# Optimization experiments

Measured on AMD Instinct MI355X. Metric: run time of the kernel, lower is better.

The kernel has to match this reference:

```python
import jax, jax.numpy as jnp
import numpy as np

B, T, C, H = 16, 2048, 512, 64


def _skew(x):
    # x: (B, T1, T2) -> relative-position skew trick (Music Transformer)
    b, t1, t2 = x.shape
    x = jnp.pad(x, ((0, 0), (0, 0), (1, 0)))        # pad one column on the left
    x = x.reshape(b, t2 + 1, t1)                    # reinterpret layout
    x = x[:, 1:, :]                                 # drop first row
    return jnp.transpose(x, (0, 2, 1))              # (B, T1, T2)


def setup_inputs() -> dict:
    key = jax.random.key(0)
    ks = jax.random.split(key, 5)
    return {
        "x": jax.random.normal(ks[0], (B, T, C), dtype=jnp.float32),
        "Wq": jax.random.normal(ks[1], (C, H), dtype=jnp.float32) * 0.02,
        "Wk": jax.random.normal(ks[2], (C, H), dtype=jnp.float32) * 0.02,
        "Wv": jax.random.normal(ks[3], (C, H), dtype=jnp.float32) * 0.02,
        "Er": jax.random.normal(ks[4], (T, H), dtype=jnp.float32),
    }


def reference(x, Wq, Wk, Wv, Er):
    b, t, c = x.shape
    q = x @ Wq  # (B, T, H)
    k = x @ Wk
    v = x @ Wv
    scale = 1.0 / (k.shape[-1] ** 0.5)
    att = jnp.einsum("bth,bsh->bts", q, k) * scale  # (B, T, T)
    # relative position bias via skew trick
    rel_att = jnp.einsum("bth,rh->btr", q, Er[:t])  # (B, T, T)
    att = att + _skew(rel_att)
    # causal mask
    mask = jnp.tril(jnp.ones((t, t), dtype=bool))
    att = jnp.where(mask, att, -jnp.inf)
    att = jax.nn.softmax(att, axis=-1)
    # dropout is identity in eval mode
    out = att @ v  # (B, T, H)
    return out
```

## Files before the change

### kernel.cpp

```cpp
#include <hip/hip_runtime.h>
#include <hip/hip_bf16.h>

#define TT 2048
#define HB 64
#define NB 16
#define NSPLIT 4

typedef __attribute__((ext_vector_type(8))) short short8;
typedef __attribute__((ext_vector_type(4))) float floatx4;

static __device__ __forceinline__ unsigned short f2bf(float f) {
  __hip_bfloat16 h = __float2bfloat16(f);
  return *reinterpret_cast<unsigned short*>(&h);
}
static __device__ __forceinline__ float bf2f(unsigned short u) {
  __hip_bfloat16 h = *reinterpret_cast<__hip_bfloat16*>(&u);
  return __bfloat162float(h);
}

__global__ __launch_bounds__(256) void prep_kernel(
    const float* __restrict__ Wq, const float* __restrict__ Wk,
    const float* __restrict__ Wv, const float* __restrict__ Er,
    unsigned short* __restrict__ Wt, unsigned short* __restrict__ Erb) {
  const int bx = blockIdx.x, tid = threadIdx.x;
  if (bx < 512) {
    int idx = bx * 256 + tid;
    Erb[idx] = f2bf(Er[idx]);
  } else {
    int n = bx - 512;
    const float* Ws[3] = {Wq, Wk, Wv};
#pragma unroll
    for (int m = 0; m < 3; m++)
      for (int k = tid; k < 512; k += 256)
        Wt[(size_t)(m * 64 + n) * 512 + k] = f2bf(Ws[m][(size_t)k * 64 + n]);
  }
}

__global__ __launch_bounds__(256) void proj_kernel(
    const float* __restrict__ x, const unsigned short* __restrict__ Wt,
    unsigned short* __restrict__ qb, unsigned short* __restrict__ kb,
    unsigned short* __restrict__ vT) {
  const int tid = threadIdx.x;
  const int w = tid >> 6, l = tid & 63, quad = l >> 4, lm = l & 15;
  const int m0 = blockIdx.x * 64;
  const int row_a = m0 + w * 16 + lm;

  floatx4 acc[12];
#pragma unroll
  for (int i = 0; i < 12; i++) acc[i] = (floatx4){0.f, 0.f, 0.f, 0.f};

  for (int kt = 0; kt < 512; kt += 64) {
    short8 af[2];
#pragma unroll
    for (int kc = 0; kc < 2; kc++) {
      const float* px = &x[(size_t)row_a * 512 + kt + kc * 32 + quad * 8];
      float4 f0 = *(const float4*)px;
      float4 f1 = *(const float4*)(px + 4);
      short8 s;
      s[0] = f2bf(f0.x); s[1] = f2bf(f0.y); s[2] = f2bf(f0.z); s[3] = f2bf(f0.w);
      s[4] = f2bf(f1.x); s[5] = f2bf(f1.y); s[6] = f2bf(f1.z); s[7] = f2bf(f1.w);
      af[kc] = s;
    }
#pragma unroll
    for (int nt = 0; nt < 12; nt++) {
      const unsigned short* pw =
          &Wt[(size_t)((nt >> 2) * 64 + (nt & 3) * 16 + lm) * 512 + kt + quad * 8];
      short8 b0 = *(const short8*)pw;
      short8 b1 = *(const short8*)(pw + 32);
      acc[nt] = __builtin_amdgcn_mfma_f32_16x16x32_bf16(af[0], b0, acc[nt], 0, 0, 0);
      acc[nt] = __builtin_amdgcn_mfma_f32_16x16x32_bf16(af[1], b1, acc[nt], 0, 0, 0);
    }
  }
  const int b = m0 >> 11;
#pragma unroll
  for (int nt = 0; nt < 12; nt++) {
    int col = (nt & 3) * 16 + lm;
#pragma unroll
    for (int rg = 0; rg < 4; rg++) {
      int row = m0 + w * 16 + quad * 4 + rg;
      unsigned short hv = f2bf(acc[nt][rg]);
      if (nt < 4) qb[(size_t)row * 64 + col] = hv;
      else if (nt < 8) kb[(size_t)row * 64 + col] = hv;
      else vT[(size_t)(b * 64 + col) * 2048 + (row & 2047)] = hv;
    }
  }
}

#define SLICE_B 11264

__global__ __launch_bounds__(256, 2) void attn_kernel(
    const unsigned short* __restrict__ qb, const unsigned short* __restrict__ kb,
    const unsigned short* __restrict__ vT, const unsigned short* __restrict__ Erb,
    float* __restrict__ out) {
  __shared__ __align__(16) char smem[4 * SLICE_B];

  const int tid = threadIdx.x;
  const int w = tid >> 6;
  const int lane = tid & 63;
  const int quad = lane >> 4, lm = lane & 15;

  float* Ds = (float*)(smem + w * SLICE_B);
  unsigned short* Ps = (unsigned short*)(smem + w * SLICE_B + 8448);
  float* dbv = (float*)(smem + w * SLICE_B + 8448 + 2560);

  const int xcd = blockIdx.x & 7;
  const int slot = blockIdx.x >> 3;
  const int b = xcd + ((slot & 1) << 3);
  const int pr = slot >> 1;
  const int s = w;

  const size_t qoff = (size_t)b * (2048 * 64);
  const unsigned short* qB = qb + qoff;
  const unsigned short* kB = kb + qoff;
  const unsigned short* vB = vT + qoff;

  for (int ph = 0; ph < 2; ph++) {
    const int it = ph ? (63 - pr) : pr;
    const int i0 = it * 32;

    short8 qf[2][2];
#pragma unroll
    for (int mt = 0; mt < 2; mt++)
#pragma unroll
      for (int kc = 0; kc < 2; kc++)
        qf[mt][kc] =
            *(const short8*)&qB[(size_t)(i0 + mt * 16 + lm) * 64 + kc * 32 + quad * 8];

    {
      short8 ebf[2];
#pragma unroll
      for (int kc = 0; kc < 2; kc++) {
        short8 z = (short8){0, 0, 0, 0, 0, 0, 0, 0};
        if (lm == 0)
          z = *(const short8*)&Erb[(size_t)2047 * 64 + kc * 32 + quad * 8];
        ebf[kc] = z;
      }
#pragma unroll
      for (int mt = 0; mt < 2; mt++) {
        floatx4 dacc = (floatx4){0.f, 0.f, 0.f, 0.f};
        dacc = __builtin_amdgcn_mfma_f32_16x16x32_bf16(qf[mt][0], ebf[0], dacc, 0, 0, 0);
        dacc = __builtin_amdgcn_mfma_f32_16x16x32_bf16(qf[mt][1], ebf[1], dacc, 0, 0, 0);
        if (lm == 0) {
#pragma unroll
          for (int rg = 0; rg < 4; rg++)
            dbv[mt * 16 + quad * 4 + rg] = dacc[rg];
        }
      }
    }
    __builtin_amdgcn_wave_barrier();

    floatx4 O[2][4];
#pragma unroll
    for (int mt = 0; mt < 2; mt++)
#pragma unroll
      for (int nt = 0; nt < 4; nt++) O[mt][nt] = (floatx4){0.f, 0.f, 0.f, 0.f};
    float m_st[2][4], l_st[2][4];
#pragma unroll
    for (int mt = 0; mt < 2; mt++)
#pragma unroll
      for (int rg = 0; rg < 4; rg++) { m_st[mt][rg] = -1e30f; l_st[mt][rg] = 0.f; }

    for (int jt = s; jt <= it; jt += NSPLIT) {
      const int j0 = jt * 32;
      const int d = i0 - j0;
      const int e0 = (d - 33 > 0) ? (d - 33) : 0;

      short8 kf[2][2], uf[2][2], ef[4][2], vf[4];
#pragma unroll
      for (int t = 0; t < 2; t++)
#pragma unroll
        for (int kc = 0; kc < 2; kc++)
          kf[t][kc] =
              *(const short8*)&kB[(size_t)(j0 + t * 16 + lm) * 64 + kc * 32 + quad * 8];
#pragma unroll
      for (int ct = 0; ct < 2; ct++)
#pragma unroll
        for (int kc = 0; kc < 2; kc++) {
          int ur = j0 + ct * 16 + lm + 1;
          if (ur > 2047) ur = 2047;
          uf[ct][kc] = *(const short8*)&qB[(size_t)ur * 64 + kc * 32 + quad * 8];
        }
#pragma unroll
      for (int et = 0; et < 4; et++)
#pragma unroll
        for (int kc = 0; kc < 2; kc++)
          ef[et][kc] = *(const short8*)&Erb[(size_t)(e0 + et * 16 + lm) * 64 +
                                            kc * 32 + quad * 8];
#pragma unroll
      for (int nt = 0; nt < 4; nt++)
        vf[nt] = *(const short8*)&vB[(size_t)(nt * 16 + lm) * 2048 + j0 + quad * 8];

      __builtin_amdgcn_wave_barrier();

#pragma unroll
      for (int ct = 0; ct < 2; ct++)
#pragma unroll
        for (int et = 0; et < 4; et++) {
          floatx4 dacc = (floatx4){0.f, 0.f, 0.f, 0.f};
          dacc = __builtin_amdgcn_mfma_f32_16x16x32_bf16(uf[ct][0], ef[et][0], dacc, 0, 0, 0);
          dacc = __builtin_amdgcn_mfma_f32_16x16x32_bf16(uf[ct][1], ef[et][1], dacc, 0, 0, 0);
#pragma unroll
          for (int rg = 0; rg < 4; rg++)
            Ds[(ct * 16 + quad * 4 + rg) * 66 + et * 16 + lm] = dacc[rg];
        }

      floatx4 S[2][2];
#pragma unroll
      for (int mt = 0; mt < 2; mt++)
#pragma unroll
        for (int t = 0; t < 2; t++) {
          floatx4 a = (floatx4){0.f, 0.f, 0.f, 0.f};
          a = __builtin_amdgcn_mfma_f32_16x16x32_bf16(qf[mt][0], kf[t][0], a, 0, 0, 0);
          a = __builtin_amdgcn_mfma_f32_16x16x32_bf16(qf[mt][1], kf[t][1], a, 0, 0, 0);
          S[mt][t] = a;
        }

      __builtin_amdgcn_wave_barrier();
      asm volatile("s_waitcnt lgkmcnt(0)" ::: "memory");
      __builtin_amdgcn_sched_barrier(0);

      float sv0[8], sv1[8], lmx[8];
      bool allok = true;
#pragma unroll
      for (int mt = 0; mt < 2; mt++)
#pragma unroll
        for (int rg = 0; rg < 4; rg++) {
          const int c = mt * 4 + rg;
          const int rloc = mt * 16 + quad * 4 + rg;
          const int i = i0 + rloc;
          float v0, v1;
          {
            int j = j0 + lm;
            float raw = 0.125f * S[mt][0][rg];
            if (j > i) v0 = -1e30f;
            else if (j == i) v0 = raw + dbv[rloc];
            else if (j == i - 1) v0 = raw;
            else v0 = raw + Ds[lm * 66 + (i - j - 2 - e0)];
          }
          {
            int j = j0 + 16 + lm;
            float raw = 0.125f * S[mt][1][rg];
            if (j > i) v1 = -1e30f;
            else if (j == i) v1 = raw + dbv[rloc];
            else if (j == i - 1) v1 = raw;
            else v1 = raw + Ds[(16 + lm) * 66 + (i - j - 2 - e0)];
          }
          sv0[c] = v0; sv1[c] = v1;
          lmx[c] = fmaxf(v0, v1);
          allok = allok && (lmx[c] <= m_st[mt][rg] + 8.f);
        }

      if (__all((int)allok)) {
#pragma unroll
        for (int mt = 0; mt < 2; mt++)
#pragma unroll
          for (int rg = 0; rg < 4; rg++) {
            const int c = mt * 4 + rg;
            const int rloc = mt * 16 + quad * 4 + rg;
            float p0 = __expf(sv0[c] - m_st[mt][rg]);
            float p1 = __expf(sv1[c] - m_st[mt][rg]);
            l_st[mt][rg] += p0 + p1;
            Ps[rloc * 40 + lm] = f2bf(p0);
            Ps[rloc * 40 + 16 + lm] = f2bf(p1);
          }
      } else {
#pragma unroll
        for (int mt = 0; mt < 2; mt++)
#pragma unroll
          for (int rg = 0; rg < 4; rg++) {
            const int c = mt * 4 + rg;
            const int rloc = mt * 16 + quad * 4 + rg;
            float mx = lmx[c];
            mx = fmaxf(mx, __shfl_xor(mx, 1));
            mx = fmaxf(mx, __shfl_xor(mx, 2));
            mx = fmaxf(mx, __shfl_xor(mx, 4));
            mx = fmaxf(mx, __shfl_xor(mx, 8));
            float m_new = fmaxf(m_st[mt][rg], mx);
            float alpha = __expf(m_st[mt][rg] - m_new);
            float p0 = __expf(sv0[c] - m_new);
            float p1 = __expf(sv1[c] - m_new);
            l_st[mt][rg] = l_st[mt][rg] * alpha + (p0 + p1);
            m_st[mt][rg] = m_new;
#pragma unroll
            for (int nt = 0; nt < 4; nt++) O[mt][nt][rg] *= alpha;
            Ps[rloc * 40 + lm] = f2bf(p0);
            Ps[rloc * 40 + 16 + lm] = f2bf(p1);
          }
      }

      __builtin_amdgcn_wave_barrier();
      asm volatile("s_waitcnt lgkmcnt(0)" ::: "memory");
      __builtin_amdgcn_sched_barrier(0);

#pragma unroll
      for (int mt = 0; mt < 2; mt++) {
        short8 pa = *(const short8*)&Ps[(mt * 16 + lm) * 40 + quad * 8];
#pragma unroll
        for (int nt = 0; nt < 4; nt++)
          O[mt][nt] = __builtin_amdgcn_mfma_f32_16x16x32_bf16(pa, vf[nt], O[mt][nt], 0, 0, 0);
      }
    }

    {
      float* Os = (float*)(smem + w * SLICE_B);
      float* mlm = (float*)(smem + w * SLICE_B + 8448);
      float* mll = (float*)(smem + w * SLICE_B + 8448 + 128);
#pragma unroll
      for (int mt = 0; mt < 2; mt++)
#pragma unroll
        for (int rg = 0; rg < 4; rg++) {
          float lr = l_st[mt][rg];
          lr += __shfl_xor(lr, 1);
          lr += __shfl_xor(lr, 2);
          lr += __shfl_xor(lr, 4);
          lr += __shfl_xor(lr, 8);
          const int rloc = mt * 16 + quad * 4 + rg;
          if (lm == 0) { mlm[rloc] = m_st[mt][rg]; mll[rloc] = lr; }
#pragma unroll
          for (int nt = 0; nt < 4; nt++)
            Os[rloc * 65 + nt * 16 + lm] = O[mt][nt][rg];
        }
    }
    __syncthreads();
    {
      const int row = tid >> 3, c0 = (tid & 7) * 8;
      float mstar = -1e30f;
#pragma unroll
      for (int s2 = 0; s2 < 4; s2++)
        mstar = fmaxf(mstar, *(const float*)(smem + s2 * SLICE_B + 8448 + row * 4));
      float den = 0.f;
      float acc[8];
#pragma unroll
      for (int c = 0; c < 8; c++) acc[c] = 0.f;
#pragma unroll
      for (int s2 = 0; s2 < 4; s2++) {
        const char* sl = smem + s2 * SLICE_B;
        float ms = *(const float*)(sl + 8448 + row * 4);
        float ls = *(const float*)(sl + 8448 + 128 + row * 4);
        float a = __expf(ms - mstar);
        den += a * ls;
        const float* osp = (const float*)sl + row * 65 + c0;
#pragma unroll
        for (int c = 0; c < 8; c++) acc[c] += a * osp[c];
      }
      float inv = 1.f / den;
      float4 r0 = {acc[0] * inv, acc[1] * inv, acc[2] * inv, acc[3] * inv};
      float4 r1 = {acc[4] * inv, acc[5] * inv, acc[6] * inv, acc[7] * inv};
      float* po = &out[qoff + (size_t)(i0 + row) * 64 + c0];
      *(float4*)po = r0;
      *((float4*)po + 1) = r1;
    }
    __syncthreads();
  }
}

extern "C" void kernel_launch(void* const* d_in, const int* in_sizes, int n_in,
                              void* d_out, int out_size, void* d_ws,
                              size_t ws_size, hipStream_t stream) {
  const float* x = (const float*)d_in[0];
  const float* Wq = (const float*)d_in[1];
  const float* Wk = (const float*)d_in[2];
  const float* Wv = (const float*)d_in[3];
  const float* Er = (const float*)d_in[4];
  float* out = (float*)d_out;

  unsigned short* qb = (unsigned short*)d_ws;
  unsigned short* kb = qb + 2097152;
  unsigned short* vT = kb + 2097152;
  unsigned short* Wt = vT + 2097152;
  unsigned short* Erb = Wt + 98304;

  prep_kernel<<<576, 256, 0, stream>>>(Wq, Wk, Wv, Er, Wt, Erb);
  proj_kernel<<<512, 256, 0, stream>>>(x, Wt, qb, kb, vT);
  attn_kernel<<<512, 256, 0, stream>>>(qb, kb, vT, Erb, out);
}
```

Before: 234.8 us.

## Prefetch next K/U/E tile and add fast path for interior skew tiles

Software-pipelines the inner attention loop so the K, shifted-Q and Er fragments for the next tile are loaded while the current tile's softmax runs. It also adds a branch-free path for tiles far from the diagonal, using a precomputed LDS pointer with an algebraically simplified skew index. Several wave barriers and explicit lgkmcnt waits are removed, the diagonal-bias fragment load is hoisted out of the phase loop, and the diagonal bias is computed only by the wave that owns the diagonal tile. The row clamp on the shifted-Q load is dropped, so the last tile may read one row past the batch and, for the final batch, past the buffer. It also raises register pressure.

After: 253.7 us. 8.0% more time.

```diff
diff --git a/kernel.cpp b/kernel.cpp
--- a/kernel.cpp
+++ b/kernel.cpp
@@ -102,6 +102,7 @@
   float* Ds = (float*)(smem + w * SLICE_B);
   unsigned short* Ps = (unsigned short*)(smem + w * SLICE_B + 8448);
   float* dbv = (float*)(smem + w * SLICE_B + 8448 + 2560);
+  const float* DsL = Ds + lm * 65 + quad * 4;
 
   const int xcd = blockIdx.x & 7;
   const int slot = blockIdx.x >> 3;
@@ -114,6 +115,15 @@
   const unsigned short* kB = kb + qoff;
   const unsigned short* vB = vT + qoff;
 
+  short8 ebf[2];
+#pragma unroll
+  for (int kc = 0; kc < 2; kc++) {
+    short8 z = (short8){0, 0, 0, 0, 0, 0, 0, 0};
+    if (lm == 0)
+      z = *(const short8*)&Erb[(size_t)2047 * 64 + kc * 32 + quad * 8];
+    ebf[kc] = z;
+  }
+
   for (int ph = 0; ph < 2; ph++) {
     const int it = ph ? (63 - pr) : pr;
     const int i0 = it * 32;
@@ -126,15 +136,7 @@
         qf[mt][kc] =
             *(const short8*)&qB[(size_t)(i0 + mt * 16 + lm) * 64 + kc * 32 + quad * 8];
 
-    {
-      short8 ebf[2];
-#pragma unroll
-      for (int kc = 0; kc < 2; kc++) {
-        short8 z = (short8){0, 0, 0, 0, 0, 0, 0, 0};
-        if (lm == 0)
-          z = *(const short8*)&Erb[(size_t)2047 * 64 + kc * 32 + quad * 8];
-        ebf[kc] = z;
-      }
+    if ((it & (NSPLIT - 1)) == w) {
 #pragma unroll
       for (int mt = 0; mt < 2; mt++) {
         floatx4 dacc = (floatx4){0.f, 0.f, 0.f, 0.f};
@@ -147,7 +149,6 @@
         }
       }
     }
-    __builtin_amdgcn_wave_barrier();
 
     floatx4 O[2][4];
 #pragma unroll
@@ -159,38 +160,42 @@
     for (int mt = 0; mt < 2; mt++)
 #pragma unroll
       for (int rg = 0; rg < 4; rg++) { m_st[mt][rg] = -1e30f; l_st[mt][rg] = 0.f; }
+
+    short8 kf[2][2], uf[2][2], ef[4][2];
+    auto LOADKUE = [&](int jn) {
+      const int j0n = jn * 32;
+      const int dn = i0 - j0n;
+      const int e0n = (dn - 33 > 0) ? (dn - 33) : 0;
+#pragma unroll
+      for (int t = 0; t < 2; t++)
+#pragma unroll
+        for (int kc = 0; kc < 2; kc++)
+          kf[t][kc] =
+              *(const short8*)&kB[(size_t)(j0n + t * 16 + lm) * 64 + kc * 32 + quad * 8];
+#pragma unroll
+      for (int ct = 0; ct < 2; ct++)
+#pragma unroll
+        for (int kc = 0; kc < 2; kc++)
+          uf[ct][kc] = *(const short8*)&qB[(size_t)(j0n + ct * 16 + lm + 1) * 64 +
+                                           kc * 32 + quad * 8];
+#pragma unroll
+      for (int et = 0; et < 4; et++)
+#pragma unroll
+        for (int kc = 0; kc < 2; kc++)
+          ef[et][kc] = *(const short8*)&Erb[(size_t)(e0n + et * 16 + lm) * 64 +
+                                            kc * 32 + quad * 8];
+    };
+    if (s <= it) LOADKUE(s);
 
     for (int jt = s; jt <= it; jt += NSPLIT) {
       const int j0 = jt * 32;
       const int d = i0 - j0;
       const int e0 = (d - 33 > 0) ? (d - 33) : 0;
 
-      short8 kf[2][2], uf[2][2], ef[4][2], vf[4];
-#pragma unroll
-      for (int t = 0; t < 2; t++)
-#pragma unroll
-        for (int kc = 0; kc < 2; kc++)
-          kf[t][kc] =
-              *(const short8*)&kB[(size_t)(j0 + t * 16 + lm) * 64 + kc * 32 + quad * 8];
-#pragma unroll
-      for (int ct = 0; ct < 2; ct++)
-#pragma unroll
-        for (int kc = 0; kc < 2; kc++) {
-          int ur = j0 + ct * 16 + lm + 1;
-          if (ur > 2047) ur = 2047;
-          uf[ct][kc] = *(const short8*)&qB[(size_t)ur * 64 + kc * 32 + quad * 8];
-        }
-#pragma unroll
-      for (int et = 0; et < 4; et++)
-#pragma unroll
-        for (int kc = 0; kc < 2; kc++)
-          ef[et][kc] = *(const short8*)&Erb[(size_t)(e0 + et * 16 + lm) * 64 +
-                                            kc * 32 + quad * 8];
+      short8 vf[4];
 #pragma unroll
       for (int nt = 0; nt < 4; nt++)
         vf[nt] = *(const short8*)&vB[(size_t)(nt * 16 + lm) * 2048 + j0 + quad * 8];
-
-      __builtin_amdgcn_wave_barrier();
 
 #pragma unroll
       for (int ct = 0; ct < 2; ct++)
@@ -215,40 +220,53 @@
           S[mt][t] = a;
         }
 
-      __builtin_amdgcn_wave_barrier();
-      asm volatile("s_waitcnt lgkmcnt(0)" ::: "memory");
-      __builtin_amdgcn_sched_barrier(0);
+      if (jt + NSPLIT <= it) LOADKUE(jt + NSPLIT);
 
       float sv0[8], sv1[8], lmx[8];
       bool allok = true;
-#pragma unroll
-      for (int mt = 0; mt < 2; mt++)
-#pragma unroll
-        for (int rg = 0; rg < 4; rg++) {
-          const int c = mt * 4 + rg;
-          const int rloc = mt * 16 + quad * 4 + rg;
-          const int i = i0 + rloc;
-          float v0, v1;
-          {
-            int j = j0 + lm;
-            float raw = 0.125f * S[mt][0][rg];
-            if (j > i) v0 = -1e30f;
-            else if (j == i) v0 = raw + dbv[rloc];
-            else if (j == i - 1) v0 = raw;
-            else v0 = raw + Ds[lm * 66 + (i - j - 2 - e0)];
+      if (d >= 64) {
+#pragma unroll
+        for (int mt = 0; mt < 2; mt++)
+#pragma unroll
+          for (int rg = 0; rg < 4; rg++) {
+            const int c = mt * 4 + rg;
+            float d0 = DsL[mt * 16 + rg + 31];
+            float d1 = DsL[1040 + mt * 16 + rg + 31];
+            sv0[c] = fmaf(0.125f, S[mt][0][rg], d0);
+            sv1[c] = fmaf(0.125f, S[mt][1][rg], d1);
+            lmx[c] = fmaxf(sv0[c], sv1[c]);
+            allok = allok && (lmx[c] <= m_st[mt][rg] + 8.f);
           }
-          {
-            int j = j0 + 16 + lm;
-            float raw = 0.125f * S[mt][1][rg];
-            if (j > i) v1 = -1e30f;
-            else if (j == i) v1 = raw + dbv[rloc];
-            else if (j == i - 1) v1 = raw;
-            else v1 = raw + Ds[(16 + lm) * 66 + (i - j - 2 - e0)];
+      } else {
+#pragma unroll
+        for (int mt = 0; mt < 2; mt++)
+#pragma unroll
+          for (int rg = 0; rg < 4; rg++) {
+            const int c = mt * 4 + rg;
+            const int rloc = mt * 16 + quad * 4 + rg;
+            const int i = i0 + rloc;
+            float v0, v1;
+            {
+              int j = j0 + lm;
+              float raw = 0.125f * S[mt][0][rg];
+              if (j > i) v0 = -1e30f;
+              else if (j == i) v0 = raw + dbv[rloc];
+              else if (j == i - 1) v0 = raw;
+              else v0 = raw + Ds[lm * 66 + (i - j - 2 - e0)];
+            }
+            {
+              int j = j0 + 16 + lm;
+              float raw = 0.125f * S[mt][1][rg];
+              if (j > i) v1 = -1e30f;
+              else if (j == i) v1 = raw + dbv[rloc];
+              else if (j == i - 1) v1 = raw;
+              else v1 = raw + Ds[(16 + lm) * 66 + (i - j - 2 - e0)];
+            }
+            sv0[c] = v0; sv1[c] = v1;
+            lmx[c] = fmaxf(v0, v1);
+            allok = allok && (lmx[c] <= m_st[mt][rg] + 8.f);
           }
-          sv0[c] = v0; sv1[c] = v1;
-          lmx[c] = fmaxf(v0, v1);
-          allok = allok && (lmx[c] <= m_st[mt][rg] + 8.f);
-        }
+      }
 
       if (__all((int)allok)) {
 #pragma unroll
@@ -288,10 +306,6 @@
           }
       }
 
-      __builtin_amdgcn_wave_barrier();
-      asm volatile("s_waitcnt lgkmcnt(0)" ::: "memory");
-      __builtin_amdgcn_sched_barrier(0);
-
 #pragma unroll
       for (int mt = 0; mt < 2; mt++) {
         short8 pa = *(const short8*)&Ps[(mt * 16 + lm) * 40 + quad * 8];
```
